# Optimization experiments

Hardware: AMD Instinct MI355X
Metric: run time of the kernel (lower is better)

Reference implementation:

```python
import jax, jax.numpy as jnp
import numpy as np

N = 2048      # nodes (= in_features = out_features, forced by h0 @ adj)
C = 512       # channels
B = 8         # batch
NNZ = 65536   # number of edges (avg degree 32)
NEG = -9e15   # masked-fill value from the source


def setup_inputs() -> dict:
    key = jax.random.key(0)
    k1, k2, k3, k4 = jax.random.split(key, 4)
    x = jax.random.normal(k1, (B, C, N), dtype=jnp.float32)
    # xavier_normal_ with gain=0.01: std = gain * sqrt(2/(fan_in+fan_out))
    std = 0.01 * float(np.sqrt(2.0 / (N + N)))
    W1 = jax.random.normal(k2, (N, N), dtype=jnp.float32) * std
    W2 = jax.random.normal(k3, (N, N), dtype=jnp.float32) * std
    # e is initialized to 1 in the source; perturb so softmax is non-trivial
    e = 1.0 + 0.1 * jax.random.normal(k4, (NNZ,), dtype=jnp.float32)
    # flat row-major indices of mask nonzeros, unique + sorted (matches adj[mask] = e)
    rng = np.random.default_rng(0)
    edge_idx = np.sort(rng.choice(N * N, size=NNZ, replace=False)).astype(np.int64)
    return {"x": x, "W1": W1, "W2": W2, "e": e, "edge_idx": jnp.asarray(edge_idx)}


def reference(x, W1, W2, e, edge_idx):
    # h0, h1: [B, C, N]
    h0 = jnp.matmul(x, W1)
    h1 = jnp.matmul(x, W2)
    # scatter per-edge logits into dense [N, N], masked positions = -9e15
    logits = jnp.full((N * N,), NEG, dtype=jnp.float32).at[edge_idx].set(e)
    A = jax.nn.softmax(logits.reshape(N, N), axis=1)  # row-wise softmax
    diag = jnp.diagonal(A)                 # A * I  (self term, diagonal scaling)
    A_off = A - jnp.diag(diag)             # A * (1 - I)  (neighbor term)
    # h0 @ (A*I) == h0 scaled per-node by diag; h1 @ (A*(1-I)) dense GEMM
    out = h0 * diag[None, None, :] + jnp.matmul(h1, A_off)
    return out  # [B, C, N]; torch squeeze is a no-op here; bias=False
```

## Files before the change

### kernel.cpp

```cpp
#include <hip/hip_runtime.h>
#include <hip/hip_bf16.h>
#include <stdint.h>

#define NN 2048
#define LOG2NN 11
#define GK 2048
#define GNC 2048

typedef __bf16 bf16x8 __attribute__((ext_vector_type(8)));
typedef float f32x4 __attribute__((ext_vector_type(4)));

__device__ __forceinline__ ushort f2bf(float f) {
  uint32_t x = __float_as_uint(f);
  uint32_t r = (x + 0x7fffu + ((x >> 16) & 1u)) >> 16;
  return (ushort)r;
}

__device__ __forceinline__ void cvt_block(const float* __restrict__ x,
                                          ushort* __restrict__ xb, int i) {
  const float4* in4 = reinterpret_cast<const float4*>(x);
  float4 a = in4[2 * i];
  float4 b = in4[2 * i + 1];
  uint4 o;
  o.x = (uint32_t)f2bf(a.x) | ((uint32_t)f2bf(a.y) << 16);
  o.y = (uint32_t)f2bf(a.z) | ((uint32_t)f2bf(a.w) << 16);
  o.z = (uint32_t)f2bf(b.x) | ((uint32_t)f2bf(b.y) << 16);
  o.w = (uint32_t)f2bf(b.z) | ((uint32_t)f2bf(b.w) << 16);
  reinterpret_cast<uint4*>(xb)[i] = o;
}

__device__ __forceinline__ int lower_bound32(const int* __restrict__ a, int n, int v) {
  int lo = 0, hi = n;
  while (lo < hi) {
    int mid = (lo + hi) >> 1;
    if (a[mid] < v) lo = mid + 1; else hi = mid;
  }
  return lo;
}

__global__ __launch_bounds__(256) void prep_kernel(
    const float* __restrict__ W1, const float* __restrict__ W2,
    ushort* __restrict__ WT, ushort* __restrict__ W2T,
    int* __restrict__ hist, int* __restrict__ ecnt,
    const int* __restrict__ idx, const float* __restrict__ e, int nnz,
    float* __restrict__ vals, float* __restrict__ diag, int* __restrict__ empty) {
  __shared__ float tile[64][65];
  const int bid = blockIdx.x;
  const int t = threadIdx.x;
  if (bid < 2048) {
    const int m = bid >> 10;
    const int rem = bid & 1023;
    const int r0 = (rem >> 5) * 64, c0 = (rem & 31) * 64;
    const float* in = m ? W2 : W1;
    ushort* out = m ? W2T : WT;
    const int tx = t & 15, ty = t >> 4;
#pragma unroll
    for (int i = 0; i < 4; ++i) {
      int r = i * 16 + ty;
      float4 v = *reinterpret_cast<const float4*>(&in[(size_t)(r0 + r) * NN + c0 + tx * 4]);
      tile[r][tx * 4 + 0] = v.x;
      tile[r][tx * 4 + 1] = v.y;
      tile[r][tx * 4 + 2] = v.z;
      tile[r][tx * 4 + 3] = v.w;
    }
    __syncthreads();
#pragma unroll
    for (int i = 0; i < 4; ++i) {
      int oc = i * 16 + ty;
      ushort4 o;
      o.x = f2bf(tile[tx * 4 + 0][oc]);
      o.y = f2bf(tile[tx * 4 + 1][oc]);
      o.z = f2bf(tile[tx * 4 + 2][oc]);
      o.w = f2bf(tile[tx * 4 + 3][oc]);
      *reinterpret_cast<ushort4*>(&out[(size_t)(c0 + oc) * NN + r0 + tx * 4]) = o;
    }
  } else {
    const int w = t >> 6, lane = t & 63;
    const int r = (bid - 2048) * 4 + w;
    int lo = lower_bound32(idx, nnz, r << LOG2NN);
    int hi = lower_bound32(idx, nnz, (r + 1) << LOG2NN);
    if (hi <= lo) {
      if (lane == 0) { diag[r] = 1.0f / NN; empty[r] = 1; atomicAdd(ecnt, 1); }
      return;
    }
    float m = -3.0e38f;
    for (int j = lo + lane; j < hi; j += 64) m = fmaxf(m, e[j]);
#pragma unroll
    for (int s = 32; s >= 1; s >>= 1) m = fmaxf(m, __shfl_xor(m, s));
    float sum = 0.f;
    for (int j = lo + lane; j < hi; j += 64) sum += expf(e[j] - m);
#pragma unroll
    for (int s = 32; s >= 1; s >>= 1) sum += __shfl_xor(sum, s);
    float inv = 1.0f / sum;
    float dv = 0.f;
    for (int j = lo + lane; j < hi; j += 64) {
      float v = expf(e[j] - m) * inv;
      vals[j] = v;
      int c = idx[j] & (NN - 1);
      if (c == r) dv = v;
      else atomicAdd(&hist[c], 1);
    }
#pragma unroll
    for (int s = 32; s >= 1; s >>= 1) dv += __shfl_xor(dv, s);
    if (lane == 0) { diag[r] = dv; empty[r] = 0; }
  }
}

__global__ __launch_bounds__(256) void scan_uw_kernel(
    const int* __restrict__ hist, int* __restrict__ base, int* __restrict__ cursor,
    const float* __restrict__ W2, const int* __restrict__ empty,
    const int* __restrict__ ecnt, float* __restrict__ uW,
    const float* __restrict__ x, ushort* __restrict__ xb) {
  if (blockIdx.x >= 9) {
    cvt_block(x, xb, ((int)blockIdx.x - 9) * 256 + threadIdx.x);
    return;
  }
  if (blockIdx.x == 0) {
    const int l = threadIdx.x;
    if (l >= 64) return;
    int vals[32], pre[32];
    int run = 0;
#pragma unroll
    for (int j = 0; j < 32; ++j) {
      vals[j] = hist[l * 32 + j];
      pre[j] = run;
      run += vals[j];
    }
    int tot = run, inc = run;
#pragma unroll
    for (int s = 1; s < 64; s <<= 1) {
      int o = __shfl_up(inc, s);
      if (l >= s) inc += o;
    }
    int excl = inc - tot;
#pragma unroll
    for (int j = 0; j < 32; ++j) {
      int b = excl + pre[j];
      base[l * 32 + j] = b;
      cursor[l * 32 + j] = b;
    }
  } else {
    if (*ecnt == 0) return;
    int p = ((int)blockIdx.x - 1) * 256 + threadIdx.x;
    float s = 0.f;
    for (int k = 0; k < NN; ++k)
      if (empty[k]) s += W2[(size_t)p * NN + k];
    uW[p] = s * (1.0f / NN);
  }
}

__global__ __launch_bounds__(256) void scatter_kernel(
    const int* __restrict__ idx, const float* __restrict__ vals,
    int nnz, int* __restrict__ cursor,
    int* __restrict__ ek, float* __restrict__ ev,
    const float* __restrict__ x, ushort* __restrict__ xb) {
  if (blockIdx.x >= 256) {
    cvt_block(x, xb, (2048 + (int)blockIdx.x - 256) * 256 + threadIdx.x);
    return;
  }
  int j = blockIdx.x * blockDim.x + threadIdx.x;
  if (j >= nnz) return;
  int f = idx[j];
  int c = f & (NN - 1), r = f >> LOG2NN;
  if (c != r) {
    int p = atomicAdd(&cursor[c], 1);
    ek[p] = r;
    ev[p] = vals[j];
  }
}

__global__ __launch_bounds__(256) void spmm_kernel(
    const int* __restrict__ ek, const float* __restrict__ ev,
    const int* __restrict__ base, const int* __restrict__ hist,
    const ushort* __restrict__ W2T,
    const float* __restrict__ diag, const int* __restrict__ empty,
    const float* __restrict__ uW, ushort* WT) {
  const int w = threadIdx.x >> 6, lane = threadIdx.x & 63;
  const int n = blockIdx.x * 2 + (w >> 1);
  const int c0 = (w & 1) * 1024 + lane * 16;
  const int start = base[n], cnt = hist[n];
  float acc[2][8];
#pragma unroll
  for (int g = 0; g < 2; ++g) {
    float4 u0 = *reinterpret_cast<const float4*>(&uW[c0 + g * 8]);
    float4 u1 = *reinterpret_cast<const float4*>(&uW[c0 + g * 8 + 4]);
    acc[g][0] = u0.x; acc[g][1] = u0.y; acc[g][2] = u0.z; acc[g][3] = u0.w;
    acc[g][4] = u1.x; acc[g][5] = u1.y; acc[g][6] = u1.z; acc[g][7] = u1.w;
  }
  float d = diag[n];
  if (d != 0.f) {
#pragma unroll
    for (int g = 0; g < 2; ++g) {
      bf16x8 wd = *reinterpret_cast<const bf16x8*>(&WT[(size_t)n * NN + c0 + g * 8]);
#pragma unroll
      for (int j = 0; j < 8; ++j) acc[g][j] += d * (float)wd[j];
    }
  }
  int i = 0;
  for (; i + 4 <= cnt; i += 4) {
    int k[4];
    float v[4];
    bf16x8 wv[4][2];
#pragma unroll
    for (int e2 = 0; e2 < 4; ++e2) {
      k[e2] = ek[start + i + e2];
      v[e2] = ev[start + i + e2];
    }
#pragma unroll
    for (int e2 = 0; e2 < 4; ++e2)
#pragma unroll
      for (int g = 0; g < 2; ++g)
        wv[e2][g] = *reinterpret_cast<const bf16x8*>(&W2T[(size_t)k[e2] * NN + c0 + g * 8]);
#pragma unroll
    for (int e2 = 0; e2 < 4; ++e2)
#pragma unroll
      for (int g = 0; g < 2; ++g)
#pragma unroll
        for (int j = 0; j < 8; ++j)
          acc[g][j] += v[e2] * (float)wv[e2][g][j];
  }
  for (; i < cnt; ++i) {
    int k0 = ek[start + i];
    float v0 = ev[start + i];
#pragma unroll
    for (int g = 0; g < 2; ++g) {
      bf16x8 w0 = *reinterpret_cast<const bf16x8*>(&W2T[(size_t)k0 * NN + c0 + g * 8]);
#pragma unroll
      for (int j = 0; j < 8; ++j) acc[g][j] += v0 * (float)w0[j];
    }
  }
  if (empty[n]) {
#pragma unroll
    for (int g = 0; g < 2; ++g) {
      bf16x8 we = *reinterpret_cast<const bf16x8*>(&W2T[(size_t)n * NN + c0 + g * 8]);
#pragma unroll
      for (int j = 0; j < 8; ++j) acc[g][j] -= (1.0f / NN) * (float)we[j];
    }
  }
#pragma unroll
  for (int g = 0; g < 2; ++g) {
    uint4 o;
    o.x = (uint32_t)f2bf(acc[g][0]) | ((uint32_t)f2bf(acc[g][1]) << 16);
    o.y = (uint32_t)f2bf(acc[g][2]) | ((uint32_t)f2bf(acc[g][3]) << 16);
    o.z = (uint32_t)f2bf(acc[g][4]) | ((uint32_t)f2bf(acc[g][5]) << 16);
    o.w = (uint32_t)f2bf(acc[g][6]) | ((uint32_t)f2bf(acc[g][7]) << 16);
    *reinterpret_cast<uint4*>(&WT[(size_t)n * NN + c0 + g * 8]) = o;
  }
}

__device__ __forceinline__ void gload_lds16(const ushort* g, char* l) {
  __builtin_amdgcn_global_load_lds(
      (__attribute__((address_space(1))) uint32_t*)(uintptr_t)g,
      (__attribute__((address_space(3))) uint32_t*)l, 16, 0, 0);
}

#define NT 32

__global__ __launch_bounds__(512, 2)
void gemm8_kernel(const ushort* __restrict__ A, const ushort* __restrict__ Bt,
                  float* __restrict__ Cf) {
  __shared__ __align__(16) char smem[147456];
  const int t = threadIdx.x;
  const int wid = t >> 6, lane = t & 63;
  const int wm = wid >> 1, wn = wid & 1;
  const int fr = lane & 15, fg = lane >> 4;

  const int swz = ((int)blockIdx.x & 7) * 32 + ((int)blockIdx.x >> 3);
  const int m0 = (swz >> 4) * 256;
  const int n0 = (swz & 15) * 128;

  const int l8 = lane >> 3;
  const int scol = ((lane & 7) ^ l8) << 3;
  const int srow = wid * 8 + l8;

#define STGA(H, TAU, BUF) do {                                                 \
    gload_lds16(A + (size_t)(m0 + (H) * 128 + srow) * GK + (TAU) * 64 + scol,  \
                smem + (BUF) * 32768 + (H) * 16384 + wid * 1024);              \
    gload_lds16(A + (size_t)(m0 + (H) * 128 + 64 + srow) * GK + (TAU) * 64 + scol, \
                smem + (BUF) * 32768 + (H) * 16384 + 8192 + wid * 1024);       \
  } while (0)

#define STGB(TAU, BUF) do {                                                    \
    gload_lds16(Bt + (size_t)(n0 + srow) * GK + (TAU) * 64 + scol,             \
                smem + 98304 + (BUF) * 16384 + wid * 1024);                    \
    gload_lds16(Bt + (size_t)(n0 + 64 + srow) * GK + (TAU) * 64 + scol,        \
                smem + 98304 + (BUF) * 16384 + 8192 + wid * 1024);             \
  } while (0)

  const int sw = (fr & 7) << 4;
  const int ko0 = (fg * 16) ^ sw;
  const int ko1 = (64 + fg * 16) ^ sw;

  f32x4 acc[4][4] = {};

  STGA(0, 0, 0); STGA(1, 0, 0); STGB(0, 0);
  STGA(0, 1, 1); STGA(1, 1, 1); STGB(1, 1);
  asm volatile("s_waitcnt vmcnt(6)" ::: "memory");
  __builtin_amdgcn_s_barrier();
  asm volatile("" ::: "memory");

  for (int kt = 0; kt < NT; ++kt) {
    const int br = kt % 3;
    const int bs = (kt + 2) % 3;
    const int t2 = (kt + 2) & (NT - 1);
    STGA(0, t2, bs); STGA(1, t2, bs); STGB(t2, bs);

    const char* Ab = smem + br * 32768;
    const char* Bb = smem + 98304 + br * 16384;
    bf16x8 aF[4][2], bF[4][2];
#pragma unroll
    for (int mf = 0; mf < 4; ++mf) {
      const int row = wm * 64 + mf * 16 + fr;
      const char* p = Ab + (row >> 7) * 16384 + (row & 127) * 128;
      aF[mf][0] = *reinterpret_cast<const bf16x8*>(p + ko0);
      aF[mf][1] = *reinterpret_cast<const bf16x8*>(p + ko1);
    }
#pragma unroll
    for (int nf = 0; nf < 4; ++nf) {
      const char* p = Bb + (wn * 64 + nf * 16 + fr) * 128;
      bF[nf][0] = *reinterpret_cast<const bf16x8*>(p + ko0);
      bF[nf][1] = *reinterpret_cast<const bf16x8*>(p + ko1);
    }
    __builtin_amdgcn_s_setprio(1);
#pragma unroll
    for (int mf = 0; mf < 4; ++mf)
#pragma unroll
      for (int nf = 0; nf < 4; ++nf)
        acc[mf][nf] = __builtin_amdgcn_mfma_f32_16x16x32_bf16(
            aF[mf][0], bF[nf][0], acc[mf][nf], 0, 0, 0);
#pragma unroll
    for (int mf = 0; mf < 4; ++mf)
#pragma unroll
      for (int nf = 0; nf < 4; ++nf)
        acc[mf][nf] = __builtin_amdgcn_mfma_f32_16x16x32_bf16(
            aF[mf][1], bF[nf][1], acc[mf][nf], 0, 0, 0);
    __builtin_amdgcn_s_setprio(0);
    asm volatile("s_waitcnt vmcnt(6)" ::: "memory");
    __builtin_amdgcn_s_barrier();
    asm volatile("" ::: "memory");
  }

  asm volatile("s_waitcnt vmcnt(0)" ::: "memory");
  const int cr = lane >> 4, cc = lane & 15;
#pragma unroll
  for (int mf = 0; mf < 4; ++mf)
#pragma unroll
    for (int nf = 0; nf < 4; ++nf)
#pragma unroll
      for (int q = 0; q < 4; ++q) {
        int gm = m0 + wm * 64 + mf * 16 + cr * 4 + q;
        int gn = n0 + wn * 64 + nf * 16 + cc;
        Cf[(size_t)gm * GNC + gn] = acc[mf][nf][q];
      }
}

extern "C" void kernel_launch(void* const* d_in, const int* in_sizes, int n_in,
                              void* d_out, int out_size, void* d_ws, size_t ws_size,
                              hipStream_t stream) {
  const float* x   = (const float*)d_in[0];
  const float* W1  = (const float*)d_in[1];
  const float* W2  = (const float*)d_in[2];
  const float* e   = (const float*)d_in[3];
  const int*   eix = (const int*)d_in[4];
  const int nnz = in_sizes[3];
  float* out = (float*)d_out;

  char* w = (char*)d_ws;
  ushort* W2T  = (ushort*)w; w += (size_t)NN * NN * 2;
  ushort* WT   = (ushort*)w; w += (size_t)NN * NN * 2;
  ushort* xb   = (ushort*)w; w += (size_t)4096 * NN * 2;
  float*  vals = (float*)w;  w += (size_t)nnz * 4;
  int*    ek   = (int*)w;    w += (size_t)nnz * 4;
  float*  ev   = (float*)w;  w += (size_t)nnz * 4;
  int*    base = (int*)w;    w += NN * 4;
  int*    curs = (int*)w;    w += NN * 4;
  float*  diag = (float*)w;  w += NN * 4;
  int*    empt = (int*)w;    w += NN * 4;
  int*    hist = (int*)w;    w += NN * 4;
  float*  uW   = (float*)w;  w += NN * 4;
  int*    ecnt = (int*)w;    w += 256;

  hipMemsetAsync(hist, 0, NN * 4 + NN * 4 + 256, stream);

  prep_kernel<<<dim3(2560), dim3(256), 0, stream>>>(W1, W2, WT, W2T,
                                                    hist, ecnt,
                                                    eix, e, nnz, vals, diag, empt);
  scan_uw_kernel<<<dim3(9 + 2048), dim3(256), 0, stream>>>(hist, base, curs, W2,
                                                           empt, ecnt, uW, x, xb);
  scatter_kernel<<<dim3(256 + 2048), dim3(256), 0, stream>>>(eix, vals, nnz, curs,
                                                             ek, ev, x, xb);
  spmm_kernel<<<dim3(1024), dim3(256), 0, stream>>>(ek, ev, base, hist, W2T,
                                                    diag, empt, uW, WT);
  gemm8_kernel<<<dim3(256), dim3(512), 0, stream>>>(xb, WT, out);
}
```

Baseline: 107.2 us.

## Switch GEMM to 32x32x16 MFMA and drop W1 transpose pass

The GEMM inner loop moves from 16x16x32 to 32x32x16 bf16 MFMA with 2x2 fragments per wave and four k-steps. This cuts LDS fragment reads per FLOP and the instruction count. The prep kernel no longer transposes and converts W1. The spmm kernel instead reads the needed W1 column entries directly in fp32 with strided gathers, which removes a full pass over a 2048x2048 matrix. The strided W1 reads in spmm are uncoalesced, and the new output index mapping must match the 32x32 accumulator layout.

```diff
diff --git a/kernel.cpp b/kernel.cpp
--- a/kernel.cpp
+++ b/kernel.cpp
@@ -9,6 +9,7 @@
 
 typedef __bf16 bf16x8 __attribute__((ext_vector_type(8)));
 typedef float f32x4 __attribute__((ext_vector_type(4)));
+typedef float f32x16 __attribute__((ext_vector_type(16)));
 
 __device__ __forceinline__ ushort f2bf(float f) {
   uint32_t x = __float_as_uint(f);
@@ -39,25 +40,20 @@
 }
 
 __global__ __launch_bounds__(256) void prep_kernel(
-    const float* __restrict__ W1, const float* __restrict__ W2,
-    ushort* __restrict__ WT, ushort* __restrict__ W2T,
+    const float* __restrict__ W2, ushort* __restrict__ W2T,
     int* __restrict__ hist, int* __restrict__ ecnt,
     const int* __restrict__ idx, const float* __restrict__ e, int nnz,
     float* __restrict__ vals, float* __restrict__ diag, int* __restrict__ empty) {
   __shared__ float tile[64][65];
   const int bid = blockIdx.x;
   const int t = threadIdx.x;
-  if (bid < 2048) {
-    const int m = bid >> 10;
-    const int rem = bid & 1023;
-    const int r0 = (rem >> 5) * 64, c0 = (rem & 31) * 64;
-    const float* in = m ? W2 : W1;
-    ushort* out = m ? W2T : WT;
+  if (bid < 1024) {
+    const int r0 = (bid >> 5) * 64, c0 = (bid & 31) * 64;
     const int tx = t & 15, ty = t >> 4;
 #pragma unroll
     for (int i = 0; i < 4; ++i) {
       int r = i * 16 + ty;
-      float4 v = *reinterpret_cast<const float4*>(&in[(size_t)(r0 + r) * NN + c0 + tx * 4]);
+      float4 v = *reinterpret_cast<const float4*>(&W2[(size_t)(r0 + r) * NN + c0 + tx * 4]);
       tile[r][tx * 4 + 0] = v.x;
       tile[r][tx * 4 + 1] = v.y;
       tile[r][tx * 4 + 2] = v.z;
@@ -72,11 +68,11 @@
       o.y = f2bf(tile[tx * 4 + 1][oc]);
       o.z = f2bf(tile[tx * 4 + 2][oc]);
       o.w = f2bf(tile[tx * 4 + 3][oc]);
-      *reinterpret_cast<ushort4*>(&out[(size_t)(c0 + oc) * NN + r0 + tx * 4]) = o;
+      *reinterpret_cast<ushort4*>(&W2T[(size_t)(c0 + oc) * NN + r0 + tx * 4]) = o;
     }
   } else {
     const int w = t >> 6, lane = t & 63;
-    const int r = (bid - 2048) * 4 + w;
+    const int r = (bid - 1024) * 4 + w;
     int lo = lower_bound32(idx, nnz, r << LOG2NN);
     int hi = lower_bound32(idx, nnz, (r + 1) << LOG2NN);
     if (hi <= lo) {
@@ -172,9 +168,9 @@
 __global__ __launch_bounds__(256) void spmm_kernel(
     const int* __restrict__ ek, const float* __restrict__ ev,
     const int* __restrict__ base, const int* __restrict__ hist,
-    const ushort* __restrict__ W2T,
+    const ushort* __restrict__ W2T, const float* __restrict__ W1,
     const float* __restrict__ diag, const int* __restrict__ empty,
-    const float* __restrict__ uW, ushort* WT) {
+    const float* __restrict__ uW, ushort* __restrict__ WT) {
   const int w = threadIdx.x >> 6, lane = threadIdx.x & 63;
   const int n = blockIdx.x * 2 + (w >> 1);
   const int c0 = (w & 1) * 1024 + lane * 16;
@@ -190,11 +186,10 @@
   float d = diag[n];
   if (d != 0.f) {
 #pragma unroll
-    for (int g = 0; g < 2; ++g) {
-      bf16x8 wd = *reinterpret_cast<const bf16x8*>(&WT[(size_t)n * NN + c0 + g * 8]);
-#pragma unroll
-      for (int j = 0; j < 8; ++j) acc[g][j] += d * (float)wd[j];
-    }
+    for (int g = 0; g < 2; ++g)
+#pragma unroll
+      for (int j = 0; j < 8; ++j)
+        acc[g][j] += d * W1[(size_t)(c0 + g * 8 + j) * NN + n];
   }
   int i = 0;
   for (; i + 4 <= cnt; i += 4) {
@@ -263,7 +258,7 @@
   const int t = threadIdx.x;
   const int wid = t >> 6, lane = t & 63;
   const int wm = wid >> 1, wn = wid & 1;
-  const int fr = lane & 15, fg = lane >> 4;
+  const int fr = lane & 31, fg = lane >> 5;
 
   const int swz = ((int)blockIdx.x & 7) * 32 + ((int)blockIdx.x >> 3);
   const int m0 = (swz >> 4) * 256;
@@ -287,11 +282,12 @@
                 smem + 98304 + (BUF) * 16384 + 8192 + wid * 1024);             \
   } while (0)
 
-  const int sw = (fr & 7) << 4;
-  const int ko0 = (fg * 16) ^ sw;
-  const int ko1 = (64 + fg * 16) ^ sw;
-
-  f32x4 acc[4][4] = {};
+  const int swb = (fr & 7) << 4;
+  int ko[4];
+#pragma unroll
+  for (int ks = 0; ks < 4; ++ks) ko[ks] = (ks * 32 + fg * 16) ^ swb;
+
+  f32x16 acc[2][2] = {};
 
   STGA(0, 0, 0); STGA(1, 0, 0); STGB(0, 0);
   STGA(0, 1, 1); STGA(1, 1, 1); STGB(1, 1);
@@ -307,33 +303,30 @@
 
     const char* Ab = smem + br * 32768;
     const char* Bb = smem + 98304 + br * 16384;
-    bf16x8 aF[4][2], bF[4][2];
-#pragma unroll
-    for (int mf = 0; mf < 4; ++mf) {
-      const int row = wm * 64 + mf * 16 + fr;
-      const char* p = Ab + (row >> 7) * 16384 + (row & 127) * 128;
-      aF[mf][0] = *reinterpret_cast<const bf16x8*>(p + ko0);
-      aF[mf][1] = *reinterpret_cast<const bf16x8*>(p + ko1);
-    }
-#pragma unroll
-    for (int nf = 0; nf < 4; ++nf) {
-      const char* p = Bb + (wn * 64 + nf * 16 + fr) * 128;
-      bF[nf][0] = *reinterpret_cast<const bf16x8*>(p + ko0);
-      bF[nf][1] = *reinterpret_cast<const bf16x8*>(p + ko1);
+    bf16x8 aF[2][4], bF[2][4];
+#pragma unroll
+    for (int ks = 0; ks < 4; ++ks) {
+#pragma unroll
+      for (int mf = 0; mf < 2; ++mf) {
+        const int row = wm * 64 + mf * 32 + fr;
+        aF[mf][ks] = *reinterpret_cast<const bf16x8*>(
+            Ab + (row >> 7) * 16384 + (row & 127) * 128 + ko[ks]);
+      }
+#pragma unroll
+      for (int nf = 0; nf < 2; ++nf) {
+        const int row = wn * 64 + nf * 32 + fr;
+        bF[nf][ks] = *reinterpret_cast<const bf16x8*>(Bb + row * 128 + ko[ks]);
+      }
     }
     __builtin_amdgcn_s_setprio(1);
 #pragma unroll
-    for (int mf = 0; mf < 4; ++mf)
-#pragma unroll
-      for (int nf = 0; nf < 4; ++nf)
-        acc[mf][nf] = __builtin_amdgcn_mfma_f32_16x16x32_bf16(
-            aF[mf][0], bF[nf][0], acc[mf][nf], 0, 0, 0);
-#pragma unroll
-    for (int mf = 0; mf < 4; ++mf)
-#pragma unroll
-      for (int nf = 0; nf < 4; ++nf)
-        acc[mf][nf] = __builtin_amdgcn_mfma_f32_16x16x32_bf16(
-            aF[mf][1], bF[nf][1], acc[mf][nf], 0, 0, 0);
+    for (int ks = 0; ks < 4; ++ks)
+#pragma unroll
+      for (int mf = 0; mf < 2; ++mf)
+#pragma unroll
+        for (int nf = 0; nf < 2; ++nf)
+          acc[mf][nf] = __builtin_amdgcn_mfma_f32_32x32x16_bf16(
+              aF[mf][ks], bF[nf][ks], acc[mf][nf], 0, 0, 0);
     __builtin_amdgcn_s_setprio(0);
     asm volatile("s_waitcnt vmcnt(6)" ::: "memory");
     __builtin_amdgcn_s_barrier();
@@ -341,15 +334,14 @@
   }
 
   asm volatile("s_waitcnt vmcnt(0)" ::: "memory");
-  const int cr = lane >> 4, cc = lane & 15;
-#pragma unroll
-  for (int mf = 0; mf < 4; ++mf)
-#pragma unroll
-    for (int nf = 0; nf < 4; ++nf)
-#pragma unroll
-      for (int q = 0; q < 4; ++q) {
-        int gm = m0 + wm * 64 + mf * 16 + cr * 4 + q;
-        int gn = n0 + wn * 64 + nf * 16 + cc;
+#pragma unroll
+  for (int mf = 0; mf < 2; ++mf)
+#pragma unroll
+    for (int nf = 0; nf < 2; ++nf)
+#pragma unroll
+      for (int q = 0; q < 16; ++q) {
+        int gm = m0 + wm * 64 + mf * 32 + (q & 3) + 8 * (q >> 2) + 4 * fg;
+        int gn = n0 + wn * 64 + nf * 32 + fr;
         Cf[(size_t)gm * GNC + gn] = acc[mf][nf][q];
       }
 }
@@ -382,14 +374,13 @@
 
   hipMemsetAsync(hist, 0, NN * 4 + NN * 4 + 256, stream);
 
-  prep_kernel<<<dim3(2560), dim3(256), 0, stream>>>(W1, W2, WT, W2T,
-                                                    hist, ecnt,
+  prep_kernel<<<dim3(1536), dim3(256), 0, stream>>>(W2, W2T, hist, ecnt,
                                                     eix, e, nnz, vals, diag, empt);
   scan_uw_kernel<<<dim3(9 + 2048), dim3(256), 0, stream>>>(hist, base, curs, W2,
                                                            empt, ecnt, uW, x, xb);
   scatter_kernel<<<dim3(256 + 2048), dim3(256), 0, stream>>>(eix, vals, nnz, curs,
                                                              ek, ev, x, xb);
-  spmm_kernel<<<dim3(1024), dim3(256), 0, stream>>>(ek, ev, base, hist, W2T,
+  spmm_kernel<<<dim3(1024), dim3(256), 0, stream>>>(ek, ev, base, hist, W2T, W1,
                                                     diag, empt, uW, WT);
   gemm8_kernel<<<dim3(256), dim3(512), 0, stream>>>(xb, WT, out);
 }
```

Result: slower. 113.7 us (+6.1%).
